# Kernel tuning notes

Hardware: AMD Instinct MI355X
Metric: run time of the kernel (lower is better)

## Reference

```python
import jax, jax.numpy as jnp
import numpy as np

BATCH = 32768
D = 1024          # vector dimension
BITS = 4          # total bit budget
MSE_BITS = BITS - 1
K = 2 ** MSE_BITS # 8 codebook centroids
QJL_DIM = D       # default qjl projection dim


def setup_inputs() -> dict:
    key = jax.random.key(0)
    kx, kq, ks = jax.random.split(key, 3)
    x = jax.random.normal(kx, (BATCH, D), dtype=jnp.float32)
    # Haar-random rotation: QR of Gaussian with sign-fixed R diagonal
    G = jax.random.normal(kq, (D, D), dtype=jnp.float32)
    Q, R = jnp.linalg.qr(G)
    s = jnp.sign(jnp.diag(R))
    s = jnp.where(s == 0, 1.0, s)
    Pi = Q * s[None, :]
    # QJL projection matrix S: iid N(0,1), shape (m, d)
    S = jax.random.normal(ks, (QJL_DIM, D), dtype=jnp.float32)
    # Lloyd-Max-style scalar codebook for N(0,1): Gaussian quantile centroids
    probs = (jnp.arange(K, dtype=jnp.float32) + 0.5) / K
    centroids = (jnp.sqrt(2.0) * jax.scipy.special.erfinv(2.0 * probs - 1.0)).astype(jnp.float32)
    return {"x": x, "Pi": Pi, "centroids": centroids, "S": S}


def reference(x, Pi, centroids, S):
    # Stage 1 (MSE quantizer): rotate, per-coordinate nearest-centroid, gather, unrotate
    y = x @ Pi.T                                   # (B, D)
    diffs = jnp.abs(y[..., None] - centroids)      # (B, D, K)
    mse_indices = jnp.argmin(diffs, axis=-1)       # (B, D) int
    y_hat = centroids[mse_indices]                 # (B, D)
    x_hat = y_hat @ Pi                             # (B, D)
    # Stage 2 (QJL on residual)
    residual = x - x_hat                           # (B, D)
    residual_norm = jnp.linalg.norm(residual, axis=-1)  # (B,)
    projected = residual @ S.T                     # (B, m)
    qjl_signs = jnp.sign(projected)
    qjl_signs = jnp.where(qjl_signs == 0, 1.0, qjl_signs)
    return mse_indices, qjl_signs, residual_norm
```

## Files before the change

kernel.cpp:

```cpp
#include <hip/hip_runtime.h>
#include <math.h>

#define B_ROWS 32768
#define DIM    1024


__device__ __forceinline__ void gemm_ABt_128x64(
    const float* __restrict__ A, const float* __restrict__ B,
    int m0, int n0, float (&accT)[8][4],
    float (*As)[132], float (*Bs)[68], int tid, int tx, int ty)
{
    const int KB[3] = {0, 512, 1024};
    for (int blk = 0; blk < 2; ++blk) {
        float accB[8][4] = {};
        for (int k0 = KB[blk]; k0 < KB[blk + 1]; k0 += 32) {
#pragma unroll
            for (int i = 0; i < 4; ++i) {
                int e = tid + 256 * i; int kq = e & 7; int r = e >> 3;
                const float4 v = *reinterpret_cast<const float4*>(&A[(size_t)(m0 + r) * DIM + k0 + kq * 4]);
                As[kq * 4 + 0][r] = v.x; As[kq * 4 + 1][r] = v.y;
                As[kq * 4 + 2][r] = v.z; As[kq * 4 + 3][r] = v.w;
            }
#pragma unroll
            for (int i = 0; i < 2; ++i) {
                int e = tid + 256 * i; int kq = e & 7; int n = e >> 3;
                const float4 v = *reinterpret_cast<const float4*>(&B[(size_t)(n0 + n) * DIM + k0 + kq * 4]);
                Bs[kq * 4 + 0][n] = v.x; Bs[kq * 4 + 1][n] = v.y;
                Bs[kq * 4 + 2][n] = v.z; Bs[kq * 4 + 3][n] = v.w;
            }
            __syncthreads();
#pragma unroll
            for (int kk = 0; kk < 32; ++kk) {
                const float4 a0 = *reinterpret_cast<const float4*>(&As[kk][ty * 8]);
                const float4 a1 = *reinterpret_cast<const float4*>(&As[kk][ty * 8 + 4]);
                const float4 bv = *reinterpret_cast<const float4*>(&Bs[kk][tx * 4]);
                const float a[8] = {a0.x, a0.y, a0.z, a0.w, a1.x, a1.y, a1.z, a1.w};
                const float b[4] = {bv.x, bv.y, bv.z, bv.w};
#pragma unroll
                for (int i = 0; i < 8; ++i)
#pragma unroll
                    for (int j = 0; j < 4; ++j)
                        accB[i][j] = fmaf(a[i], b[j], accB[i][j]);
            }
            __syncthreads();
        }
#pragma unroll
        for (int i = 0; i < 8; ++i)
#pragma unroll
            for (int j = 0; j < 4; ++j)
                accT[i][j] = (blk == 0) ? accB[i][j] : (accT[i][j] + accB[i][j]);
    }
}

__global__ __launch_bounds__(256) void k1_rot_quant(
    const float* __restrict__ X, const float* __restrict__ Pi, const float* __restrict__ C,
    float* __restrict__ idxf, unsigned char* __restrict__ idx8)
{
    __shared__ float As[32][132];
    __shared__ float Bs[32][68];
    const int tid = threadIdx.x, tx = tid & 15, ty = tid >> 4;
    const int m0 = blockIdx.y * 128, n0 = blockIdx.x * 64;
    float accT[8][4];
    gemm_ABt_128x64(X, Pi, m0, n0, accT, As, Bs, tid, tx, ty);
    float c8[8];
#pragma unroll
    for (int t = 0; t < 8; ++t) c8[t] = C[t];
#pragma unroll
    for (int i = 0; i < 8; ++i) {
        const size_t o = (size_t)(m0 + ty * 8 + i) * DIM + n0 + tx * 4;
        float fv[4]; unsigned char bv[4];
#pragma unroll
        for (int j = 0; j < 4; ++j) {
            const float y = accT[i][j];
            float best = fabsf(y - c8[0]); int bi = 0;
#pragma unroll
            for (int t = 1; t < 8; ++t) {
                const float d = fabsf(y - c8[t]);
                if (d < best) { best = d; bi = t; }
            }
            fv[j] = (float)bi; bv[j] = (unsigned char)bi;
        }
        *reinterpret_cast<float4*>(&idxf[o]) = make_float4(fv[0], fv[1], fv[2], fv[3]);
        *reinterpret_cast<uchar4*>(&idx8[o]) = make_uchar4(bv[0], bv[1], bv[2], bv[3]);
    }
}

__global__ __launch_bounds__(256) void k3_unrot_residual(
    const float* __restrict__ X, const float* __restrict__ Pi, const float* __restrict__ C,
    const unsigned char* __restrict__ idx8, float* __restrict__ R)
{
    __shared__ float As[32][132];
    __shared__ float Bs[32][68];
    __shared__ float clut[8];
    const int tid = threadIdx.x, tx = tid & 15, ty = tid >> 4;
    if (tid < 8) clut[tid] = C[tid];
    __syncthreads();
    const int m0 = blockIdx.y * 128, n0 = blockIdx.x * 64;
    const int KB[3] = {0, 512, 1024};
    float accT[8][4];
    for (int blk = 0; blk < 2; ++blk) {
        float accB[8][4] = {};
        for (int k0 = KB[blk]; k0 < KB[blk + 1]; k0 += 32) {
#pragma unroll
            for (int i = 0; i < 4; ++i) {
                int e = tid + 256 * i; int kq = e & 7; int r = e >> 3;
                const uchar4 v = *reinterpret_cast<const uchar4*>(&idx8[(size_t)(m0 + r) * DIM + k0 + kq * 4]);
                As[kq * 4 + 0][r] = clut[v.x]; As[kq * 4 + 1][r] = clut[v.y];
                As[kq * 4 + 2][r] = clut[v.z]; As[kq * 4 + 3][r] = clut[v.w];
            }
#pragma unroll
            for (int i = 0; i < 2; ++i) {
                int e = tid + 256 * i; int nq = e & 15; int kr = e >> 4;
                const float4 v = *reinterpret_cast<const float4*>(&Pi[(size_t)(k0 + kr) * DIM + n0 + nq * 4]);
                *reinterpret_cast<float4*>(&Bs[kr][nq * 4]) = v;
            }
            __syncthreads();
#pragma unroll
            for (int kk = 0; kk < 32; ++kk) {
                const float4 a0 = *reinterpret_cast<const float4*>(&As[kk][ty * 8]);
                const float4 a1 = *reinterpret_cast<const float4*>(&As[kk][ty * 8 + 4]);
                const float4 bv = *reinterpret_cast<const float4*>(&Bs[kk][tx * 4]);
                const float a[8] = {a0.x, a0.y, a0.z, a0.w, a1.x, a1.y, a1.z, a1.w};
                const float b[4] = {bv.x, bv.y, bv.z, bv.w};
#pragma unroll
                for (int i = 0; i < 8; ++i)
#pragma unroll
                    for (int j = 0; j < 4; ++j)
                        accB[i][j] = fmaf(a[i], b[j], accB[i][j]);
            }
            __syncthreads();
        }
#pragma unroll
        for (int i = 0; i < 8; ++i)
#pragma unroll
            for (int j = 0; j < 4; ++j)
                accT[i][j] = (blk == 0) ? accB[i][j] : (accT[i][j] + accB[i][j]);
    }
#pragma unroll
    for (int i = 0; i < 8; ++i) {
        const size_t o = (size_t)(m0 + ty * 8 + i) * DIM + n0 + tx * 4;
        const float4 xv = *reinterpret_cast<const float4*>(&X[o]);
        *reinterpret_cast<float4*>(&R[o]) =
            make_float4(xv.x - accT[i][0], xv.y - accT[i][1], xv.z - accT[i][2], xv.w - accT[i][3]);
    }
}

__global__ __launch_bounds__(256) void k4_norms(const float* __restrict__ R, float* __restrict__ outn)
{
    const int row = blockIdx.x;
    const float4 v = *reinterpret_cast<const float4*>(&R[(size_t)row * DIM + threadIdx.x * 4]);
    double s = (double)v.x * v.x;
    s = fma((double)v.y, (double)v.y, s);
    s = fma((double)v.z, (double)v.z, s);
    s = fma((double)v.w, (double)v.w, s);
#pragma unroll
    for (int off = 32; off; off >>= 1) s += __shfl_down(s, off);
    __shared__ double wsum[4];
    if ((threadIdx.x & 63) == 0) wsum[threadIdx.x >> 6] = s;
    __syncthreads();
    if (threadIdx.x == 0)
        outn[row] = (float)sqrt(wsum[0] + wsum[1] + wsum[2] + wsum[3]);
}

__global__ __launch_bounds__(256) void k5_qjl(
    const float* __restrict__ R, const float* __restrict__ S, float* __restrict__ sgn)
{
    __shared__ float As[32][132];
    __shared__ float Bs[32][68];
    const int tid = threadIdx.x, tx = tid & 15, ty = tid >> 4;
    const int m0 = blockIdx.y * 128, n0 = blockIdx.x * 64;
    float accT[8][4];
    gemm_ABt_128x64(R, S, m0, n0, accT, As, Bs, tid, tx, ty);
#pragma unroll
    for (int i = 0; i < 8; ++i) {
        const size_t o = (size_t)(m0 + ty * 8 + i) * DIM + n0 + tx * 4;
        *reinterpret_cast<float4*>(&sgn[o]) = make_float4(
            (accT[i][0] >= 0.f) ? 1.f : -1.f, (accT[i][1] >= 0.f) ? 1.f : -1.f,
            (accT[i][2] >= 0.f) ? 1.f : -1.f, (accT[i][3] >= 0.f) ? 1.f : -1.f);
    }
}

extern "C" void kernel_launch(void* const* d_in, const int* in_sizes, int n_in,
                              void* d_out, int out_size, void* d_ws, size_t ws_size,
                              hipStream_t stream) {
    const float* X  = (const float*)d_in[0];
    const float* Pi = (const float*)d_in[1];
    const float* C  = (const float*)d_in[2];
    const float* S  = (const float*)d_in[3];

    float* out  = (float*)d_out;
    float* idxf = out;
    float* sgn  = out + (size_t)B_ROWS * DIM;
    float* nrm  = sgn + (size_t)B_ROWS * DIM;

    char* ws = (char*)d_ws;
    float*         R    = (float*)ws;
    unsigned char* idx8 = (unsigned char*)(ws + (size_t)B_ROWS * DIM * sizeof(float));

    dim3 blk(256);
    dim3 gG(DIM / 64, B_ROWS / 128);

    k1_rot_quant     <<<gG, blk, 0, stream>>>(X, Pi, C, idxf, idx8);
    k3_unrot_residual<<<gG, blk, 0, stream>>>(X, Pi, C, idx8, R);
    k4_norms         <<<B_ROWS, blk, 0, stream>>>(R, nrm);
    k5_qjl           <<<gG, blk, 0, stream>>>(R, S, sgn);
}
```

Measured before the change: 2.740 ms.

## Register-prefetch GEMM tiles, swizzle LDS layout, fuse residual norm via atomics

Result: slower. 6.286 ms (+129.4%).

```diff
diff --git a/kernel.cpp b/kernel.cpp
--- a/kernel.cpp
+++ b/kernel.cpp
@@ -3,65 +3,83 @@
 
 #define B_ROWS 32768
 #define DIM    1024
-
-
-__device__ __forceinline__ void gemm_ABt_128x64(
-    const float* __restrict__ A, const float* __restrict__ B,
-    int m0, int n0, float (&accT)[8][4],
-    float (*As)[132], float (*Bs)[68], int tid, int tx, int ty)
-{
-    const int KB[3] = {0, 512, 1024};
-    for (int blk = 0; blk < 2; ++blk) {
-        float accB[8][4] = {};
-        for (int k0 = KB[blk]; k0 < KB[blk + 1]; k0 += 32) {
-#pragma unroll
-            for (int i = 0; i < 4; ++i) {
-                int e = tid + 256 * i; int kq = e & 7; int r = e >> 3;
-                const float4 v = *reinterpret_cast<const float4*>(&A[(size_t)(m0 + r) * DIM + k0 + kq * 4]);
-                As[kq * 4 + 0][r] = v.x; As[kq * 4 + 1][r] = v.y;
-                As[kq * 4 + 2][r] = v.z; As[kq * 4 + 3][r] = v.w;
-            }
-#pragma unroll
-            for (int i = 0; i < 2; ++i) {
-                int e = tid + 256 * i; int kq = e & 7; int n = e >> 3;
-                const float4 v = *reinterpret_cast<const float4*>(&B[(size_t)(n0 + n) * DIM + k0 + kq * 4]);
-                Bs[kq * 4 + 0][n] = v.x; Bs[kq * 4 + 1][n] = v.y;
-                Bs[kq * 4 + 2][n] = v.z; Bs[kq * 4 + 3][n] = v.w;
-            }
-            __syncthreads();
-#pragma unroll
-            for (int kk = 0; kk < 32; ++kk) {
-                const float4 a0 = *reinterpret_cast<const float4*>(&As[kk][ty * 8]);
-                const float4 a1 = *reinterpret_cast<const float4*>(&As[kk][ty * 8 + 4]);
-                const float4 bv = *reinterpret_cast<const float4*>(&Bs[kk][tx * 4]);
-                const float a[8] = {a0.x, a0.y, a0.z, a0.w, a1.x, a1.y, a1.z, a1.w};
-                const float b[4] = {bv.x, bv.y, bv.z, bv.w};
-#pragma unroll
-                for (int i = 0; i < 8; ++i)
-#pragma unroll
-                    for (int j = 0; j < 4; ++j)
-                        accB[i][j] = fmaf(a[i], b[j], accB[i][j]);
-            }
-            __syncthreads();
-        }
+#define PA 132
+#define PB 68
+
+
+struct FragT { float4 a0, a1, a2, a3, b0, b1; };
+struct FragN { uchar4 a0, a1, a2, a3; float4 b0, b1; };
+
+__device__ __forceinline__ void loadT(const float* pA, const float* pB, FragT& f) {
+    f.a0 = *(const float4*)(pA);
+    f.a1 = *(const float4*)(pA + 32 * DIM);
+    f.a2 = *(const float4*)(pA + 64 * DIM);
+    f.a3 = *(const float4*)(pA + 96 * DIM);
+    f.b0 = *(const float4*)(pB);
+    f.b1 = *(const float4*)(pB + 32 * DIM);
+}
+
+__device__ __forceinline__ void storeT(const FragT& f, float (*As)[PA], float (*Bs)[PB],
+                                       int kq, int r0) {
+    const int c0 = kq * 4, hh = kq & 3;
+#pragma unroll
+    for (int i = 0; i < 4; ++i) {
+        const float4 v = (i == 0) ? f.a0 : (i == 1) ? f.a1 : (i == 2) ? f.a2 : f.a3;
+        const int r = r0 + 32 * i;
+        const int col = (((r >> 3) + hh) & 15) * 8 + (r & 7);
+        As[c0 + 0][col] = v.x; As[c0 + 1][col] = v.y;
+        As[c0 + 2][col] = v.z; As[c0 + 3][col] = v.w;
+    }
+#pragma unroll
+    for (int i = 0; i < 2; ++i) {
+        const float4 v = (i == 0) ? f.b0 : f.b1;
+        const int n = r0 + 32 * i;
+        const int col = (((n >> 3) + hh) & 7) * 8 + (n & 7);
+        Bs[c0 + 0][col] = v.x; Bs[c0 + 1][col] = v.y;
+        Bs[c0 + 2][col] = v.z; Bs[c0 + 3][col] = v.w;
+    }
+}
+
+__device__ __forceinline__ void computeT(const float (*As)[PA], const float (*Bs)[PB],
+                                         int tx, int ty, float (&acc)[8][4]) {
+#pragma unroll
+    for (int kk = 0; kk < 32; ++kk) {
+        const int h = (kk >> 2) & 3;
+        const float4 a0 = *(const float4*)&As[kk][((ty + h) & 15) * 8];
+        const float4 a1 = *(const float4*)&As[kk][((ty + h) & 15) * 8 + 4];
+        const float4 bv = *(const float4*)&Bs[kk][(((tx >> 1) + h) & 7) * 8 + (tx & 1) * 4];
+        const float a[8] = {a0.x, a0.y, a0.z, a0.w, a1.x, a1.y, a1.z, a1.w};
+        const float b[4] = {bv.x, bv.y, bv.z, bv.w};
 #pragma unroll
         for (int i = 0; i < 8; ++i)
 #pragma unroll
             for (int j = 0; j < 4; ++j)
-                accT[i][j] = (blk == 0) ? accB[i][j] : (accT[i][j] + accB[i][j]);
-    }
-}
-
-__global__ __launch_bounds__(256) void k1_rot_quant(
+                acc[i][j] = fmaf(a[i], b[j], acc[i][j]);
+    }
+}
+
+__global__ __launch_bounds__(256, 4) void k1_rot_quant(
     const float* __restrict__ X, const float* __restrict__ Pi, const float* __restrict__ C,
     float* __restrict__ idxf, unsigned char* __restrict__ idx8)
 {
-    __shared__ float As[32][132];
-    __shared__ float Bs[32][68];
+    __shared__ float As[32][PA];
+    __shared__ float Bs[32][PB];
     const int tid = threadIdx.x, tx = tid & 15, ty = tid >> 4;
+    const int kq = tid & 7, r0 = tid >> 3;
     const int m0 = blockIdx.y * 128, n0 = blockIdx.x * 64;
-    float accT[8][4];
-    gemm_ABt_128x64(X, Pi, m0, n0, accT, As, Bs, tid, tx, ty);
+    const float* pA = X  + (size_t)(m0 + r0) * DIM + kq * 4;
+    const float* pB = Pi + (size_t)(n0 + r0) * DIM + kq * 4;
+    float acc1[8][4] = {}, acc2[8][4] = {};
+    FragT f;
+    loadT(pA, pB, f);
+    for (int t = 0; t < 32; ++t) {
+        __syncthreads();
+        storeT(f, As, Bs, kq, r0);
+        __syncthreads();
+        if (t < 31) loadT(pA + (t + 1) * 32, pB + (t + 1) * 32, f);
+        if (t < 16) computeT(As, Bs, tx, ty, acc1);
+        else        computeT(As, Bs, tx, ty, acc2);
+    }
     float c8[8];
 #pragma unroll
     for (int t = 0; t < 8; ++t) c8[t] = C[t];
@@ -71,113 +89,148 @@
         float fv[4]; unsigned char bv[4];
 #pragma unroll
         for (int j = 0; j < 4; ++j) {
-            const float y = accT[i][j];
+            const float y = acc1[i][j] + acc2[i][j];
             float best = fabsf(y - c8[0]); int bi = 0;
 #pragma unroll
-            for (int t = 1; t < 8; ++t) {
-                const float d = fabsf(y - c8[t]);
-                if (d < best) { best = d; bi = t; }
+            for (int t2 = 1; t2 < 8; ++t2) {
+                const float d = fabsf(y - c8[t2]);
+                if (d < best) { best = d; bi = t2; }
             }
             fv[j] = (float)bi; bv[j] = (unsigned char)bi;
         }
-        *reinterpret_cast<float4*>(&idxf[o]) = make_float4(fv[0], fv[1], fv[2], fv[3]);
-        *reinterpret_cast<uchar4*>(&idx8[o]) = make_uchar4(bv[0], bv[1], bv[2], bv[3]);
-    }
-}
-
-__global__ __launch_bounds__(256) void k3_unrot_residual(
+        *(float4*)&idxf[o] = make_float4(fv[0], fv[1], fv[2], fv[3]);
+        *(uchar4*)&idx8[o] = make_uchar4(bv[0], bv[1], bv[2], bv[3]);
+    }
+}
+
+__device__ __forceinline__ void storeN(const FragN& f, const float* clut,
+                                       float (*As)[PA], float (*Bs)[PB],
+                                       int kq, int r0, int nq, int kr0) {
+    const int c0 = kq * 4, hh = kq & 3;
+#pragma unroll
+    for (int i = 0; i < 4; ++i) {
+        const uchar4 v = (i == 0) ? f.a0 : (i == 1) ? f.a1 : (i == 2) ? f.a2 : f.a3;
+        const int r = r0 + 32 * i;
+        const int col = (((r >> 3) + hh) & 15) * 8 + (r & 7);
+        As[c0 + 0][col] = clut[v.x]; As[c0 + 1][col] = clut[v.y];
+        As[c0 + 2][col] = clut[v.z]; As[c0 + 3][col] = clut[v.w];
+    }
+    *(float4*)&Bs[kr0][nq * 4]      = f.b0;
+    *(float4*)&Bs[kr0 + 16][nq * 4] = f.b1;
+}
+
+__global__ __launch_bounds__(256, 4) void k3_unrot_residual(
     const float* __restrict__ X, const float* __restrict__ Pi, const float* __restrict__ C,
-    const unsigned char* __restrict__ idx8, float* __restrict__ R)
-{
-    __shared__ float As[32][132];
-    __shared__ float Bs[32][68];
+    const unsigned char* __restrict__ idx8, float* __restrict__ R, double* __restrict__ nrm2)
+{
+    __shared__ float As[32][PA];
+    __shared__ float Bs[32][PB];
     __shared__ float clut[8];
     const int tid = threadIdx.x, tx = tid & 15, ty = tid >> 4;
+    const int kq = tid & 7, r0 = tid >> 3;
+    const int nq = tid & 15, kr0 = tid >> 4;
+    const int m0 = blockIdx.y * 128, n0 = blockIdx.x * 64;
     if (tid < 8) clut[tid] = C[tid];
-    __syncthreads();
+    const unsigned char* pA = idx8 + (size_t)(m0 + r0) * DIM + kq * 4;
+    const float*         pB = Pi + (size_t)kr0 * DIM + n0 + nq * 4;
+    float acc1[8][4] = {}, acc2[8][4] = {};
+    FragN f;
+    f.a0 = *(const uchar4*)(pA);
+    f.a1 = *(const uchar4*)(pA + 32 * DIM);
+    f.a2 = *(const uchar4*)(pA + 64 * DIM);
+    f.a3 = *(const uchar4*)(pA + 96 * DIM);
+    f.b0 = *(const float4*)(pB);
+    f.b1 = *(const float4*)(pB + 16 * DIM);
+    for (int t = 0; t < 32; ++t) {
+        __syncthreads();
+        storeN(f, clut, As, Bs, kq, r0, nq, kr0);
+        __syncthreads();
+        if (t < 31) {
+            const unsigned char* qA = pA + (t + 1) * 32;
+            const float* qB = pB + (size_t)(t + 1) * 32 * DIM;
+            f.a0 = *(const uchar4*)(qA);
+            f.a1 = *(const uchar4*)(qA + 32 * DIM);
+            f.a2 = *(const uchar4*)(qA + 64 * DIM);
+            f.a3 = *(const uchar4*)(qA + 96 * DIM);
+            f.b0 = *(const float4*)(qB);
+            f.b1 = *(const float4*)(qB + 16 * DIM);
+        }
+#pragma unroll
+        for (int kk = 0; kk < 32; ++kk) {
+            const int h = (kk >> 2) & 3;
+            const float4 a0 = *(const float4*)&As[kk][((ty + h) & 15) * 8];
+            const float4 a1 = *(const float4*)&As[kk][((ty + h) & 15) * 8 + 4];
+            const float4 bv = *(const float4*)&Bs[kk][tx * 4];
+            const float a[8] = {a0.x, a0.y, a0.z, a0.w, a1.x, a1.y, a1.z, a1.w};
+            const float b[4] = {bv.x, bv.y, bv.z, bv.w};
+            if (t < 16) {
+#pragma unroll
+                for (int i = 0; i < 8; ++i)
+#pragma unroll
+                    for (int j = 0; j < 4; ++j) acc1[i][j] = fmaf(a[i], b[j], acc1[i][j]);
+            } else {
+#pragma unroll
+                for (int i = 0; i < 8; ++i)
+#pragma unroll
+                    for (int j = 0; j < 4; ++j) acc2[i][j] = fmaf(a[i], b[j], acc2[i][j]);
+            }
+        }
+    }
+#pragma unroll
+    for (int i = 0; i < 8; ++i) {
+        const int row = m0 + ty * 8 + i;
+        const size_t o = (size_t)row * DIM + n0 + tx * 4;
+        const float4 xv = *(const float4*)&X[o];
+        const float r0v = xv.x - (acc1[i][0] + acc2[i][0]);
+        const float r1v = xv.y - (acc1[i][1] + acc2[i][1]);
+        const float r2v = xv.z - (acc1[i][2] + acc2[i][2]);
+        const float r3v = xv.w - (acc1[i][3] + acc2[i][3]);
+        *(float4*)&R[o] = make_float4(r0v, r1v, r2v, r3v);
+        double s = (double)r0v * r0v;
+        s = fma((double)r1v, (double)r1v, s);
+        s = fma((double)r2v, (double)r2v, s);
+        s = fma((double)r3v, (double)r3v, s);
+#pragma unroll
+        for (int mask = 1; mask < 16; mask <<= 1) s += __shfl_xor(s, mask, 16);
+        if (tx == 0) atomicAdd(&nrm2[row], s);
+    }
+}
+
+__global__ __launch_bounds__(256, 4) void k5_qjl(
+    const float* __restrict__ R, const float* __restrict__ S, float* __restrict__ sgn)
+{
+    __shared__ float As[32][PA];
+    __shared__ float Bs[32][PB];
+    const int tid = threadIdx.x, tx = tid & 15, ty = tid >> 4;
+    const int kq = tid & 7, r0 = tid >> 3;
     const int m0 = blockIdx.y * 128, n0 = blockIdx.x * 64;
-    const int KB[3] = {0, 512, 1024};
-    float accT[8][4];
-    for (int blk = 0; blk < 2; ++blk) {
-        float accB[8][4] = {};
-        for (int k0 = KB[blk]; k0 < KB[blk + 1]; k0 += 32) {
-#pragma unroll
-            for (int i = 0; i < 4; ++i) {
-                int e = tid + 256 * i; int kq = e & 7; int r = e >> 3;
-                const uchar4 v = *reinterpret_cast<const uchar4*>(&idx8[(size_t)(m0 + r) * DIM + k0 + kq * 4]);
-                As[kq * 4 + 0][r] = clut[v.x]; As[kq * 4 + 1][r] = clut[v.y];
-                As[kq * 4 + 2][r] = clut[v.z]; As[kq * 4 + 3][r] = clut[v.w];
-            }
-#pragma unroll
-            for (int i = 0; i < 2; ++i) {
-                int e = tid + 256 * i; int nq = e & 15; int kr = e >> 4;
-                const float4 v = *reinterpret_cast<const float4*>(&Pi[(size_t)(k0 + kr) * DIM + n0 + nq * 4]);
-                *reinterpret_cast<float4*>(&Bs[kr][nq * 4]) = v;
-            }
-            __syncthreads();
-#pragma unroll
-            for (int kk = 0; kk < 32; ++kk) {
-                const float4 a0 = *reinterpret_cast<const float4*>(&As[kk][ty * 8]);
-                const float4 a1 = *reinterpret_cast<const float4*>(&As[kk][ty * 8 + 4]);
-                const float4 bv = *reinterpret_cast<const float4*>(&Bs[kk][tx * 4]);
-                const float a[8] = {a0.x, a0.y, a0.z, a0.w, a1.x, a1.y, a1.z, a1.w};
-                const float b[4] = {bv.x, bv.y, bv.z, bv.w};
-#pragma unroll
-                for (int i = 0; i < 8; ++i)
-#pragma unroll
-                    for (int j = 0; j < 4; ++j)
-                        accB[i][j] = fmaf(a[i], b[j], accB[i][j]);
-            }
-            __syncthreads();
-        }
-#pragma unroll
-        for (int i = 0; i < 8; ++i)
-#pragma unroll
-            for (int j = 0; j < 4; ++j)
-                accT[i][j] = (blk == 0) ? accB[i][j] : (accT[i][j] + accB[i][j]);
+    const float* pA = R + (size_t)(m0 + r0) * DIM + kq * 4;
+    const float* pB = S + (size_t)(n0 + r0) * DIM + kq * 4;
+    float acc1[8][4] = {}, acc2[8][4] = {};
+    FragT f;
+    loadT(pA, pB, f);
+    for (int t = 0; t < 32; ++t) {
+        __syncthreads();
+        storeT(f, As, Bs, kq, r0);
+        __syncthreads();
+        if (t < 31) loadT(pA + (t + 1) * 32, pB + (t + 1) * 32, f);
+        if (t < 16) computeT(As, Bs, tx, ty, acc1);
+        else        computeT(As, Bs, tx, ty, acc2);
     }
 #pragma unroll
     for (int i = 0; i < 8; ++i) {
         const size_t o = (size_t)(m0 + ty * 8 + i) * DIM + n0 + tx * 4;
-        const float4 xv = *reinterpret_cast<const float4*>(&X[o]);
-        *reinterpret_cast<float4*>(&R[o]) =
-            make_float4(xv.x - accT[i][0], xv.y - accT[i][1], xv.z - accT[i][2], xv.w - accT[i][3]);
-    }
-}
-
-__global__ __launch_bounds__(256) void k4_norms(const float* __restrict__ R, float* __restrict__ outn)
-{
-    const int row = blockIdx.x;
-    const float4 v = *reinterpret_cast<const float4*>(&R[(size_t)row * DIM + threadIdx.x * 4]);
-    double s = (double)v.x * v.x;
-    s = fma((double)v.y, (double)v.y, s);
-    s = fma((double)v.z, (double)v.z, s);
-    s = fma((double)v.w, (double)v.w, s);
-#pragma unroll
-    for (int off = 32; off; off >>= 1) s += __shfl_down(s, off);
-    __shared__ double wsum[4];
-    if ((threadIdx.x & 63) == 0) wsum[threadIdx.x >> 6] = s;
-    __syncthreads();
-    if (threadIdx.x == 0)
-        outn[row] = (float)sqrt(wsum[0] + wsum[1] + wsum[2] + wsum[3]);
-}
-
-__global__ __launch_bounds__(256) void k5_qjl(
-    const float* __restrict__ R, const float* __restrict__ S, float* __restrict__ sgn)
-{
-    __shared__ float As[32][132];
-    __shared__ float Bs[32][68];
-    const int tid = threadIdx.x, tx = tid & 15, ty = tid >> 4;
-    const int m0 = blockIdx.y * 128, n0 = blockIdx.x * 64;
-    float accT[8][4];
-    gemm_ABt_128x64(R, S, m0, n0, accT, As, Bs, tid, tx, ty);
-#pragma unroll
-    for (int i = 0; i < 8; ++i) {
-        const size_t o = (size_t)(m0 + ty * 8 + i) * DIM + n0 + tx * 4;
-        *reinterpret_cast<float4*>(&sgn[o]) = make_float4(
-            (accT[i][0] >= 0.f) ? 1.f : -1.f, (accT[i][1] >= 0.f) ? 1.f : -1.f,
-            (accT[i][2] >= 0.f) ? 1.f : -1.f, (accT[i][3] >= 0.f) ? 1.f : -1.f);
-    }
+        const float p0 = acc1[i][0] + acc2[i][0], p1 = acc1[i][1] + acc2[i][1];
+        const float p2 = acc1[i][2] + acc2[i][2], p3 = acc1[i][3] + acc2[i][3];
+        *(float4*)&sgn[o] = make_float4((p0 >= 0.f) ? 1.f : -1.f, (p1 >= 0.f) ? 1.f : -1.f,
+                                        (p2 >= 0.f) ? 1.f : -1.f, (p3 >= 0.f) ? 1.f : -1.f);
+    }
+}
+
+__global__ __launch_bounds__(256) void kN_sqrt(const double* __restrict__ nrm2, float* __restrict__ nrm)
+{
+    const int i = blockIdx.x * 256 + threadIdx.x;
+    if (i < B_ROWS) nrm[i] = (float)sqrt(nrm2[i]);
 }
 
 extern "C" void kernel_launch(void* const* d_in, const int* in_sizes, int n_in,
@@ -195,13 +248,16 @@
 
     char* ws = (char*)d_ws;
     float*         R    = (float*)ws;
-    unsigned char* idx8 = (unsigned char*)(ws + (size_t)B_ROWS * DIM * sizeof(float));
+    unsigned char* idx8 = (unsigned char*)(ws + (size_t)B_ROWS * DIM * 4);
+    double*        nrm2 = (double*)(ws + (size_t)B_ROWS * DIM * 5);
+
+    hipMemsetAsync(nrm2, 0, (size_t)B_ROWS * sizeof(double), stream);
 
     dim3 blk(256);
     dim3 gG(DIM / 64, B_ROWS / 128);
 
     k1_rot_quant     <<<gG, blk, 0, stream>>>(X, Pi, C, idxf, idx8);
-    k3_unrot_residual<<<gG, blk, 0, stream>>>(X, Pi, C, idx8, R);
-    k4_norms         <<<B_ROWS, blk, 0, stream>>>(R, nrm);
+    k3_unrot_residual<<<gG, blk, 0, stream>>>(X, Pi, C, idx8, R, nrm2);
+    kN_sqrt          <<<dim3(B_ROWS / 256), blk, 0, stream>>>(nrm2, nrm);
     k5_qjl           <<<gG, blk, 0, stream>>>(R, S, sgn);
 }
```
